# Kernel optimization log

Measured on AMD Instinct MI355X. Metric: run time of the kernel, lower is better.

The kernel has to match this reference:

```python
import jax, jax.numpy as jnp
import numpy as np

HEADS = 8


def setup_inputs() -> dict:
    key = jax.random.key(0)
    ks = jax.random.split(key, 6)
    dim = 256
    s = 0.02
    return {
        "x": jax.random.normal(ks[0], (8, dim, 32, 32), jnp.float32),
        "w_qkv": jax.random.normal(ks[1], (3 * dim, dim), jnp.float32) * s,
        "w_out": jax.random.normal(ks[2], (dim, dim), jnp.float32) * s,
        "b_out": jnp.zeros((dim,), jnp.float32),
        "w_g1": jax.random.normal(ks[3], (dim // 4, dim), jnp.float32) * s,
        "b_g1": jnp.zeros((dim // 4,), jnp.float32),
        "w_g2": jax.random.normal(ks[4], (1, dim // 4), jnp.float32) * s,
        "b_g2": jnp.zeros((1,), jnp.float32),
    }


def _conv1x1(t, w, bias=None):
    # 1x1 conv == channel matmul
    y = jnp.einsum('bchw,oc->bohw', t, w)
    if bias is not None:
        y = y + bias[None, :, None, None]
    return y


def _forward(x, w_qkv, w_out, b_out, w_g1, b_g1, w_g2, b_g2):
    b, c, h, w = x.shape
    heads = HEADS
    d = c // heads
    n = h * w
    m = min(h, w)
    scale = d ** (-0.5)

    qkv = _conv1x1(x, w_qkv)  # [b, 3c, h, w]

    def to_heads(t):  # 'b (h d) x y -> b h (x y) d'
        return t.reshape(b, heads, d, n).transpose(0, 1, 3, 2)

    q, k, v = (to_heads(t) for t in jnp.split(qkv, 3, axis=1))

    attn = jax.nn.softmax(jnp.einsum('bhid,bhjd->bhij', q, k) * scale, axis=-1)

    # diagonal branch (anti-diagonal scores are computed in the original but
    # never used in the output -> omitted as dead code)
    q2d = q.reshape(b, heads, h, w, d)
    k2d = k.reshape(b, heads, h, w, d)
    q_dm = jnp.diagonal(q2d, axis1=2, axis2=3)  # [b, heads, d, m]
    k_dm = jnp.diagonal(k2d, axis1=2, axis2=3)
    diag_main = jnp.einsum('bhnd,bhmd->bhnm', q_dm, k_dm) * scale  # [b, heads, d, d]
    diag_vec = jnp.diagonal(diag_main.mean(axis=1), axis1=-2, axis2=-1)  # [b, d]
    diag_vec = jnp.pad(diag_vec, ((0, 0), (0, n - m)))  # [b, n] (d == m)

    DIAG_WEIGHT = 0.3
    enhanced = attn + DIAG_WEIGHT * diag_vec[:, None, :, None]

    out = jnp.einsum('bhij,bhjd->bhid', enhanced, v)  # [b, heads, n, d]
    out = out.reshape(b, heads, h, w, d).transpose(0, 1, 4, 2, 3).reshape(b, c, h, w)

    # left/right asymmetry gate
    mid = w // 2
    left = x[:, :, :, :mid]
    right = x[:, :, :, mid:]
    asym = jnp.abs(left - right[:, :, :, ::-1])  # [b, c, h, w/2]
    # adaptive_avg_pool2d (h, w/2) -> (h, w) with even w == width repeat by 2
    pooled = jnp.repeat(asym, 2, axis=3)
    g = _conv1x1(pooled, w_g1, b_g1)
    g = jax.nn.gelu(g, approximate=False)
    g = jax.nn.sigmoid(_conv1x1(g, w_g2, b_g2))  # [b, 1, h, w]

    out = out * (1.0 + g)
    return _conv1x1(out, w_out, b_out)


def reference(x, w_qkv, w_out, b_out, w_g1, b_g1, w_g2, b_g2):
    return _forward(x, w_qkv, w_out, b_out, w_g1, b_g1, w_g2, b_g2)
```

## Files before the change

kernel.cpp:

```cpp
#include <hip/hip_runtime.h>
#include <hip/hip_bf16.h>
#include <math.h>

#define B 8
#define C 256
#define HEADS 8
#define D 32
#define NPIX 1024
#define OC 768
#define SCALE 0.17677669529663687f
#define LOG2E 1.4426950408889634f

typedef unsigned int uint;
typedef unsigned short u16;
typedef __attribute__((ext_vector_type(8))) short bf16x8;
typedef __attribute__((ext_vector_type(4))) short bf16x4;
typedef __attribute__((ext_vector_type(4))) float f32x4;

static __device__ inline u16 f2bf(float f) {
  uint u = __float_as_uint(f);
  return (u16)((u + 0x7fffu + ((u >> 16) & 1u)) >> 16);
}
static __device__ inline float bfval(u16 v) { return __uint_as_float((uint)v << 16); }
static __device__ inline float bf_lo(uint u) { return __uint_as_float(u << 16); }
static __device__ inline float bf_hi(uint u) { return __uint_as_float(u & 0xffff0000u); }

static __device__ inline uint pk2(float lo, float hi) {
  union { __hip_bfloat162 h; uint u; } cv;
  cv.h = __float22bfloat162_rn(float2{lo, hi});
  return cv.u;
}

__global__ __launch_bounds__(256) void k_prep(
    const float* __restrict__ x, const float* __restrict__ wqkv,
    const float* __restrict__ wout,
    u16* __restrict__ WQ, u16* __restrict__ WO, u16* __restrict__ XT) {
  const int bid = blockIdx.x, t = threadIdx.x;
  __shared__ u16 tile[64][65];
  if (bid < 256) {
    const float* src;
    u16* dst;
    int base;
    if (bid < 192) { src = wqkv; dst = WQ; base = bid * 1024; }
    else           { src = wout; dst = WO; base = (bid - 192) * 1024; }
    float4 v = *(const float4*)(src + base + t * 4);
    uint2 pk = make_uint2((uint)f2bf(v.x) | ((uint)f2bf(v.y) << 16),
                          (uint)f2bf(v.z) | ((uint)f2bf(v.w) << 16));
    *(uint2*)(dst + base + t * 4) = pk;
    return;
  }
  const int id = bid - 256;
  const int pt = id & 15, ct = (id >> 4) & 3, b = id >> 6;
  {
    const int px = t & 63, cq = t >> 6;
    const float* xb = x + ((size_t)(b * C + ct * 64)) * NPIX + pt * 64;
#pragma unroll
    for (int m = 0; m < 16; ++m) {
      const int c = cq * 16 + m;
      tile[c][px] = f2bf(xb[(size_t)c * NPIX + px]);
    }
  }
  __syncthreads();
  {
    const int cc = t & 63, pq = t >> 6;
    const int c = ct * 64 + cc;
    const int kc = c >> 5, quad = (c >> 3) & 3, mm = c & 7;
    u16* dst = XT + ((size_t)((b * 64 + pt * 4 + pq) * 8 + kc) * 512 +
                     quad * 128 + mm);
#pragma unroll
    for (int m = 0; m < 16; ++m)
      dst[m * 8] = tile[cc][pq * 16 + m];
  }
}

__global__ __launch_bounds__(256) void k_qkv_mfma(
    const u16* __restrict__ XTF, const u16* __restrict__ WQ,
    u16* __restrict__ Q, u16* __restrict__ Kk, u16* __restrict__ VT) {
  const int ob = blockIdx.x, pb = blockIdx.y, b = blockIdx.z;
  const int wv = threadIdx.x >> 6, lane = threadIdx.x & 63;
  const int quad = lane >> 4, l15 = lane & 15;
  const int part = ob >> 2;
  const int odl = (ob & 3) * 64 + wv * 16;
  const int hh = odl >> 5, d0 = odl & 31;
  const int bh = b * HEADS + hh;
  const int pix0 = pb * 128;

  const u16* arow = WQ + (size_t)(ob * 64 + wv * 16 + l15) * C;
  bf16x8 af[8];
#pragma unroll
  for (int kc = 0; kc < 8; ++kc)
    af[kc] = *(const bf16x8*)(arow + kc * 32 + quad * 8);

  const u16* xb = XTF + (size_t)(b * 64 + pb * 8) * 8 * 512 + lane * 8;
  f32x4 acc[8];
#pragma unroll
  for (int nt = 0; nt < 8; ++nt) acc[nt] = (f32x4){0.f, 0.f, 0.f, 0.f};

  for (int kc = 0; kc < 8; ++kc) {
#pragma unroll
    for (int nt = 0; nt < 8; ++nt) {
      bf16x8 bfr = *(const bf16x8*)(xb + (size_t)(nt * 8 + kc) * 512);
      acc[nt] = __builtin_amdgcn_mfma_f32_16x16x32_bf16(af[kc], bfr, acc[nt], 0, 0, 0);
    }
  }

  if (part == 0) {
    const float qs = SCALE * LOG2E;
    u16* dst = Q + (size_t)bh * NPIX * D;
#pragma unroll
    for (int nt = 0; nt < 8; ++nt) {
      const int pix = pix0 + nt * 16 + l15;
      uint2 pk = make_uint2(
          (uint)f2bf(acc[nt][0] * qs) | ((uint)f2bf(acc[nt][1] * qs) << 16),
          (uint)f2bf(acc[nt][2] * qs) | ((uint)f2bf(acc[nt][3] * qs) << 16));
      *(uint2*)(dst + (size_t)pix * D + d0 + 4 * quad) = pk;
    }
  } else if (part == 1) {
    u16* kfb = Kk + (size_t)bh * NPIX * D;
    const int lane_k8 = (((d0 >> 3) + (quad >> 1)) * 16 + l15) * 8 + (quad & 1) * 4;
#pragma unroll
    for (int nt = 0; nt < 8; ++nt) {
      uint2 pk = make_uint2(
          (uint)f2bf(acc[nt][0]) | ((uint)f2bf(acc[nt][1]) << 16),
          (uint)f2bf(acc[nt][2]) | ((uint)f2bf(acc[nt][3]) << 16));
      *(uint2*)(kfb + (size_t)(pb * 8 + nt) * 512 + lane_k8) = pk;
    }
  } else {
    u16* vb = VT + (size_t)bh * NPIX * D;
#pragma unroll
    for (int nt = 0; nt < 8; ++nt) {
      const int pix = pix0 + nt * 16 + l15;
      const int jb16 = pix >> 4, qa = (pix >> 2) & 3, m = pix & 3;
#pragma unroll
      for (int r = 0; r < 4; ++r) {
        const int d = d0 + 4 * quad + r;
        const int nta = d >> 4, l15a = d & 15;
        vb[((size_t)(jb16 * 2 + nta) * 64 + qa * 16 + l15a) * 4 + m] =
            f2bf(acc[nt][r]);
      }
    }
  }
}

__global__ __launch_bounds__(256) void k_red(
    const u16* __restrict__ Q, const u16* __restrict__ KF,
    const u16* __restrict__ VT, float* __restrict__ diagv,
    float* __restrict__ colsum) {
  const int bid = blockIdx.x, tid = threadIdx.x;
  __shared__ float red[256];
  if (bid < 8) {
    const int b = bid;
    const int hh = tid >> 5, dd = tid & 31;
    const u16* qb = Q + (size_t)(b * HEADS + hh) * NPIX * D;
    const u16* kb = KF + (size_t)(b * HEADS + hh) * NPIX * D;
    float s = 0.f;
#pragma unroll 4
    for (int t = 0; t < 32; ++t) {
      const int j = t * 33;
      float qv = bfval(qb[(size_t)j * D + dd]);
      float kv = bfval(kb[(size_t)(j >> 4) * 512 +
                          ((dd >> 3) * 16 + (j & 15)) * 8 + (dd & 7)]);
      s += qv * kv;
    }
    red[tid] = s;
    __syncthreads();
    if (tid < 32) {
      float v = 0.f;
#pragma unroll
      for (int h8 = 0; h8 < 8; ++h8) v += red[h8 * 32 + tid];
      diagv[b * 32 + tid] = v * (0.125f / LOG2E);
    }
  } else {
    const int bh = bid - 8;
    const int d = tid >> 3, sl = tid & 7;
    const int nta = d >> 4, l15a = d & 15;
    const u16* vb = VT + (size_t)bh * NPIX * D;
    float s = 0.f;
    for (int jb = 0; jb < 8; ++jb) {
      const int jb16 = sl * 8 + jb;
#pragma unroll
      for (int qa = 0; qa < 4; ++qa) {
        const uint2 u = *(const uint2*)(
            vb + ((size_t)(jb16 * 2 + nta) * 64 + qa * 16 + l15a) * 4);
        s += bf_lo(u.x) + bf_hi(u.x) + bf_lo(u.y) + bf_hi(u.y);
      }
    }
    red[tid] = s;
    __syncthreads();
    if (tid < 32) {
      float v = 0.f;
#pragma unroll
      for (int g = 0; g < 8; ++g) v += red[tid * 8 + g];
      colsum[bh * D + tid] = v;
    }
  }
}

__global__ __launch_bounds__(512, 4) void k_attn(
    const u16* __restrict__ Q, const u16* __restrict__ KF,
    const u16* __restrict__ VF, const float* __restrict__ diagv,
    const float* __restrict__ colsum, u16* __restrict__ AOT) {
  const int qc = blockIdx.x;
  const int bh = blockIdx.y;
  const int b = bh >> 3, hh = bh & 7;
  const int wv = threadIdx.x >> 6, lane = threadIdx.x & 63;
  const int quad = lane >> 4, l15 = lane & 15;
  const int i0 = qc * 128 + wv * 16;

  __shared__ u16 sbuf[2][4096];

  const u16* Qb  = Q  + (size_t)bh * NPIX * D;
  const u16* KFb = KF + (size_t)bh * NPIX * D;
  const u16* VFb = VF + (size_t)bh * NPIX * D;

  bf16x8 qfrag = *(const bf16x8*)(Qb + (size_t)(i0 + l15) * D + quad * 8);

  f32x4 oacc[2];
  oacc[0] = (f32x4){0.f, 0.f, 0.f, 0.f};
  oacc[1] = (f32x4){0.f, 0.f, 0.f, 0.f};
  float lacc[4] = {};

  const int soff = (wv >= 4 ? 2048 : 0) + (wv & 3) * 512 + lane * 8;
  const u16* gsrc = (wv < 4 ? KFb : VFb) + (wv & 3) * 512 + lane * 8;
  u16* ldst[2] = { &sbuf[0][soff], &sbuf[1][soff] };

  *(uint4*)(ldst[0]) = *(const uint4*)(gsrc);
  __syncthreads();

  int cur = 0;
  for (int it = 0; it < 16; ++it) {
    if (it < 15)
      *(uint4*)(ldst[cur ^ 1]) = *(const uint4*)(gsrc + (size_t)(it + 1) * 2048);
    const u16* sK = &sbuf[cur][0];
    const u16* sV = &sbuf[cur][2048];

    f32x4 st[4];
#pragma unroll
    for (int jt = 0; jt < 4; ++jt) {
      bf16x8 kfrag = *(const bf16x8*)(sK + jt * 512 + lane * 8);
      st[jt] = __builtin_amdgcn_mfma_f32_16x16x32_bf16(
          kfrag, qfrag, (f32x4){0.f, 0.f, 0.f, 0.f}, 0, 0, 0);
    }

#pragma unroll
    for (int jt = 0; jt < 4; ++jt)
#pragma unroll
      for (int r = 0; r < 4; ++r) {
        float pv = exp2f(fminf(st[jt][r], 80.f));
        lacc[r] += pv;
        st[jt][r] = pv;
      }

    __builtin_amdgcn_s_setprio(1);
#pragma unroll
    for (int jt = 0; jt < 4; ++jt) {
      union { uint u[2]; bf16x4 v; } pa;
      pa.u[0] = pk2(st[jt][0], st[jt][1]);
      pa.u[1] = pk2(st[jt][2], st[jt][3]);
#pragma unroll
      for (int nt = 0; nt < 2; ++nt) {
        bf16x4 vfr = *(const bf16x4*)(sV + (jt * 2 + nt) * 256 + lane * 4);
        oacc[nt] = __builtin_amdgcn_mfma_f32_16x16x16bf16_1k(
            pa.v, vfr, oacc[nt], 0, 0, 0);
      }
    }
    __builtin_amdgcn_s_setprio(0);

    __syncthreads();
    cur ^= 1;
  }

  float lt = (lacc[0] + lacc[1]) + (lacc[2] + lacc[3]);
  lt += __shfl_xor(lt, 16, 64);
  lt += __shfl_xor(lt, 32, 64);
  const float linv = 1.f / lt;
  float rinv[4];
#pragma unroll
  for (int r = 0; r < 4; ++r) rinv[r] = __shfl(linv, quad * 4 + r, 64);

  const bool do_diag = (i0 < 32);
#pragma unroll
  for (int nt = 0; nt < 2; ++nt) {
    const int dch = hh * 32 + nt * 16 + l15;
    float cs = do_diag ? colsum[bh * D + (nt * 16 + l15)] : 0.f;
#pragma unroll
    for (int r = 0; r < 4; ++r) {
      const int irow = i0 + quad * 4 + r;
      float o = oacc[nt][r] * rinv[r];
      if (do_diag) o += 0.3f * diagv[b * 32 + irow] * cs;
      AOT[((size_t)b * NPIX + irow) * C + dch] = f2bf(o);
    }
  }
}

__global__ __launch_bounds__(256) void k_gate(
    const float* __restrict__ x,
    const float* __restrict__ wg1, const float* __restrict__ bg1,
    const float* __restrict__ wg2, const float* __restrict__ bg2,
    float* __restrict__ gate) {
  const int h = blockIdx.x, b = blockIdx.y, tid = threadIdx.x;
  __shared__ float pl[16 * 257];
  __shared__ float gl[16 * 65];

  {
    const int c = tid;
    const float* row = x + ((size_t)(b * C + c) * NPIX + h * 32);
    float v[32];
#pragma unroll
    for (int m = 0; m < 32; ++m) v[m] = row[m];
#pragma unroll
    for (int k = 0; k < 16; ++k) pl[k * 257 + c] = fabsf(v[k] - v[31 - k]);
  }
  __syncthreads();

  const int o16 = tid >> 4, k = tid & 15;
#pragma unroll 1
  for (int p = 0; p < 4; ++p) {
    const int o = p * 16 + o16;
    const float* wr = wg1 + o * C;
    float a0 = 0.f, a1 = 0.f, a2 = 0.f, a3 = 0.f;
#pragma unroll 4
    for (int c = 0; c < C; c += 4) {
      a0 += wr[c]     * pl[k * 257 + c];
      a1 += wr[c + 1] * pl[k * 257 + c + 1];
      a2 += wr[c + 2] * pl[k * 257 + c + 2];
      a3 += wr[c + 3] * pl[k * 257 + c + 3];
    }
    float a = bg1[o] + ((a0 + a1) + (a2 + a3));
    gl[k * 65 + o] = 0.5f * a * (1.f + erff(a * 0.70710678118654752f));
  }
  __syncthreads();

  if (tid < 16) {
    float s = bg2[0];
    for (int o = 0; o < 64; ++o)
      s += wg2[o] * gl[tid * 65 + o];
    gate[(b * 32 + h) * 16 + tid] = 1.f / (1.f + expf(-s));
  }
}

__global__ __launch_bounds__(256) void k_out_mfma(
    const u16* __restrict__ AOT, const u16* __restrict__ WO,
    const float* __restrict__ bout, const float* __restrict__ gate,
    float* __restrict__ out) {
  const int ob = blockIdx.x, pb = blockIdx.y, b = blockIdx.z;
  const int wv = threadIdx.x >> 6, lane = threadIdx.x & 63;
  const int quad = lane >> 4, l15 = lane & 15;
  const int o0 = ob * 64 + wv * 16;
  const int pix0 = pb * 128;

  const u16* arow = WO + (size_t)(o0 + l15) * C;
  bf16x8 af[8];
#pragma unroll
  for (int kc = 0; kc < 8; ++kc)
    af[kc] = *(const bf16x8*)(arow + kc * 32 + quad * 8);

  const u16* ab = AOT + (size_t)(b * NPIX + pix0) * C;
  f32x4 acc[8];
#pragma unroll
  for (int nt = 0; nt < 8; ++nt) acc[nt] = (f32x4){0.f, 0.f, 0.f, 0.f};

  for (int kc = 0; kc < 8; ++kc) {
#pragma unroll
    for (int nt = 0; nt < 8; ++nt) {
      bf16x8 bfr = *(const bf16x8*)(ab + (size_t)(nt * 16 + l15) * C +
                                    kc * 32 + quad * 8);
      acc[nt] = __builtin_amdgcn_mfma_f32_16x16x32_bf16(af[kc], bfr, acc[nt], 0, 0, 0);
    }
  }

#pragma unroll
  for (int nt = 0; nt < 8; ++nt) {
    const int pix = pix0 + nt * 16 + l15;
    const float gf = 1.f + gate[(b * 32 + (pix >> 5)) * 16 + ((pix & 31) >> 1)];
#pragma unroll
    for (int r = 0; r < 4; ++r) {
      const int o = o0 + 4 * quad + r;
      out[((size_t)b * C + o) * NPIX + pix] = acc[nt][r] * gf + bout[o];
    }
  }
}

extern "C" void kernel_launch(void* const* d_in, const int* in_sizes, int n_in,
                              void* d_out, int out_size, void* d_ws, size_t ws_size,
                              hipStream_t stream) {
  const float* x    = (const float*)d_in[0];
  const float* wqkv = (const float*)d_in[1];
  const float* wout = (const float*)d_in[2];
  const float* bout = (const float*)d_in[3];
  const float* wg1  = (const float*)d_in[4];
  const float* bg1  = (const float*)d_in[5];
  const float* wg2  = (const float*)d_in[6];
  const float* bg2  = (const float*)d_in[7];
  float* out = (float*)d_out;

  const size_t SZ = (size_t)B * HEADS * NPIX * D;
  u16* XT = (u16*)d_ws;
  u16* WQ = XT + SZ;
  u16* WO = WQ + (size_t)OC * C;
  u16* Q  = WO + (size_t)C * C;
  u16* Kq = Q + SZ;
  u16* VT = Kq + SZ;
  float* DIAG = (float*)(VT + SZ);
  float* COL  = DIAG + 256;
  float* GATE = COL + 2048;
  u16* AOT = XT;

  hipLaunchKernelGGL(k_prep, dim3(768), dim3(256), 0, stream,
                     x, wqkv, wout, WQ, WO, XT);
  hipLaunchKernelGGL(k_qkv_mfma, dim3(12, 8, B), dim3(256), 0, stream,
                     XT, WQ, Q, Kq, VT);
  hipLaunchKernelGGL(k_red, dim3(72), dim3(256), 0, stream,
                     Q, Kq, VT, DIAG, COL);
  hipLaunchKernelGGL(k_attn, dim3(8, 64), dim3(512), 0, stream,
                     Q, Kq, VT, DIAG, COL, AOT);
  hipLaunchKernelGGL(k_gate, dim3(32, B), dim3(256), 0, stream,
                     x, wg1, bg1, wg2, bg2, GATE);
  hipLaunchKernelGGL(k_out_mfma, dim3(4, 8, B), dim3(256), 0, stream,
                     AOT, WO, bout, GATE, out);
}
```

Baseline: 156.4 us.

## Fuse gate computation into prep kernel and write attention output in MFMA fragment layout

The gate kernel is merged into the prep kernel as an extra 256 blocks, removing one launch and letting gate work overlap with the weight conversion and transpose. The attention kernel now stores its bf16 output directly in the MFMA-fragment-tiled layout, so the output projection loads each fragment as one contiguous 16-byte read per lane instead of strided row reads. The attention output stores become scattered 2-byte writes, and the prep kernel's shared-memory footprint grows to the gate's size.

Measured after the change: 147.8 us. 5.5% less time.

```diff
diff --git a/kernel.cpp b/kernel.cpp
--- a/kernel.cpp
+++ b/kernel.cpp
@@ -31,12 +31,15 @@
   return cv.u;
 }
 
-__global__ __launch_bounds__(256) void k_prep(
+__global__ __launch_bounds__(256) void k_prep_gate(
     const float* __restrict__ x, const float* __restrict__ wqkv,
     const float* __restrict__ wout,
-    u16* __restrict__ WQ, u16* __restrict__ WO, u16* __restrict__ XT) {
+    const float* __restrict__ wg1, const float* __restrict__ bg1,
+    const float* __restrict__ wg2, const float* __restrict__ bg2,
+    u16* __restrict__ WQ, u16* __restrict__ WO, u16* __restrict__ XT,
+    float* __restrict__ gate) {
   const int bid = blockIdx.x, t = threadIdx.x;
-  __shared__ u16 tile[64][65];
+  __shared__ float smem[16 * 257 + 16 * 65];
   if (bid < 256) {
     const float* src;
     u16* dst;
@@ -49,27 +52,70 @@
     *(uint2*)(dst + base + t * 4) = pk;
     return;
   }
-  const int id = bid - 256;
-  const int pt = id & 15, ct = (id >> 4) & 3, b = id >> 6;
+  if (bid < 768) {
+    u16 (*tile)[65] = (u16(*)[65])smem;
+    const int id = bid - 256;
+    const int pt = id & 15, ct = (id >> 4) & 3, b = id >> 6;
+    {
+      const int px = t & 63, cq = t >> 6;
+      const float* xb = x + ((size_t)(b * C + ct * 64)) * NPIX + pt * 64;
+#pragma unroll
+      for (int m = 0; m < 16; ++m) {
+        const int c = cq * 16 + m;
+        tile[c][px] = f2bf(xb[(size_t)c * NPIX + px]);
+      }
+    }
+    __syncthreads();
+    {
+      const int cc = t & 63, pq = t >> 6;
+      const int c = ct * 64 + cc;
+      const int kc = c >> 5, quad = (c >> 3) & 3, mm = c & 7;
+      u16* dst = XT + ((size_t)((b * 64 + pt * 4 + pq) * 8 + kc) * 512 +
+                       quad * 128 + mm);
+#pragma unroll
+      for (int m = 0; m < 16; ++m)
+        dst[m * 8] = tile[cc][pq * 16 + m];
+    }
+    return;
+  }
+  const int id = bid - 768;
+  const int h = id & 31, b = id >> 5;
+  float* pl = smem;
+  float* gl = smem + 16 * 257;
   {
-    const int px = t & 63, cq = t >> 6;
-    const float* xb = x + ((size_t)(b * C + ct * 64)) * NPIX + pt * 64;
-#pragma unroll
-    for (int m = 0; m < 16; ++m) {
-      const int c = cq * 16 + m;
-      tile[c][px] = f2bf(xb[(size_t)c * NPIX + px]);
-    }
+    const int c = t;
+    const float* row = x + ((size_t)(b * C + c) * NPIX + h * 32);
+    float v[32];
+#pragma unroll
+    for (int m = 0; m < 32; ++m) v[m] = row[m];
+#pragma unroll
+    for (int k = 0; k < 16; ++k) pl[k * 257 + c] = fabsf(v[k] - v[31 - k]);
   }
   __syncthreads();
-  {
-    const int cc = t & 63, pq = t >> 6;
-    const int c = ct * 64 + cc;
-    const int kc = c >> 5, quad = (c >> 3) & 3, mm = c & 7;
-    u16* dst = XT + ((size_t)((b * 64 + pt * 4 + pq) * 8 + kc) * 512 +
-                     quad * 128 + mm);
-#pragma unroll
-    for (int m = 0; m < 16; ++m)
-      dst[m * 8] = tile[cc][pq * 16 + m];
+
+  const int o16 = t >> 4, k = t & 15;
+#pragma unroll 1
+  for (int p = 0; p < 4; ++p) {
+    const int o = p * 16 + o16;
+    const float* wr = wg1 + o * C;
+    float a0 = 0.f, a1 = 0.f, a2 = 0.f, a3 = 0.f;
+#pragma unroll 4
+    for (int c = 0; c < C; c += 4) {
+      a0 += wr[c]     * pl[k * 257 + c];
+      a1 += wr[c + 1] * pl[k * 257 + c + 1];
+      a2 += wr[c + 2] * pl[k * 257 + c + 2];
+      a3 += wr[c + 3] * pl[k * 257 + c + 3];
+    }
+    float a = bg1[o] + ((a0 + a1) + (a2 + a3));
+    gl[k * 65 + o] = 0.5f * a * (1.f + erff(a * 0.70710678118654752f));
+  }
+  __syncthreads();
+
+  if (t < 16) {
+    float s = bg2[0];
+    for (int o = 0; o < 64; ++o)
+      s += wg2[o] * gl[t * 65 + o];
+    gate[(b * 32 + h) * 16 + t] = 1.f / (1.f + expf(-s));
   }
 }
 
@@ -279,68 +325,25 @@
   for (int r = 0; r < 4; ++r) rinv[r] = __shfl(linv, quad * 4 + r, 64);
 
   const bool do_diag = (i0 < 32);
+  const int p16 = i0 >> 4;
+  u16* aobase = AOT + ((size_t)(b * 64 + p16) * 8 + hh) * 512 + (l15 & 7);
+  const int hi8 = l15 >> 3;
 #pragma unroll
   for (int nt = 0; nt < 2; ++nt) {
-    const int dch = hh * 32 + nt * 16 + l15;
+    const int qa = nt * 2 + hi8;
     float cs = do_diag ? colsum[bh * D + (nt * 16 + l15)] : 0.f;
 #pragma unroll
     for (int r = 0; r < 4; ++r) {
       const int irow = i0 + quad * 4 + r;
       float o = oacc[nt][r] * rinv[r];
       if (do_diag) o += 0.3f * diagv[b * 32 + irow] * cs;
-      AOT[((size_t)b * NPIX + irow) * C + dch] = f2bf(o);
-    }
-  }
-}
-
-__global__ __launch_bounds__(256) void k_gate(
-    const float* __restrict__ x,
-    const float* __restrict__ wg1, const float* __restrict__ bg1,
-    const float* __restrict__ wg2, const float* __restrict__ bg2,
-    float* __restrict__ gate) {
-  const int h = blockIdx.x, b = blockIdx.y, tid = threadIdx.x;
-  __shared__ float pl[16 * 257];
-  __shared__ float gl[16 * 65];
-
-  {
-    const int c = tid;
-    const float* row = x + ((size_t)(b * C + c) * NPIX + h * 32);
-    float v[32];
-#pragma unroll
-    for (int m = 0; m < 32; ++m) v[m] = row[m];
-#pragma unroll
-    for (int k = 0; k < 16; ++k) pl[k * 257 + c] = fabsf(v[k] - v[31 - k]);
-  }
-  __syncthreads();
-
-  const int o16 = tid >> 4, k = tid & 15;
-#pragma unroll 1
-  for (int p = 0; p < 4; ++p) {
-    const int o = p * 16 + o16;
-    const float* wr = wg1 + o * C;
-    float a0 = 0.f, a1 = 0.f, a2 = 0.f, a3 = 0.f;
-#pragma unroll 4
-    for (int c = 0; c < C; c += 4) {
-      a0 += wr[c]     * pl[k * 257 + c];
-      a1 += wr[c + 1] * pl[k * 257 + c + 1];
-      a2 += wr[c + 2] * pl[k * 257 + c + 2];
-      a3 += wr[c + 3] * pl[k * 257 + c + 3];
-    }
-    float a = bg1[o] + ((a0 + a1) + (a2 + a3));
-    gl[k * 65 + o] = 0.5f * a * (1.f + erff(a * 0.70710678118654752f));
-  }
-  __syncthreads();
-
-  if (tid < 16) {
-    float s = bg2[0];
-    for (int o = 0; o < 64; ++o)
-      s += wg2[o] * gl[tid * 65 + o];
-    gate[(b * 32 + h) * 16 + tid] = 1.f / (1.f + expf(-s));
+      aobase[(qa * 16 + quad * 4 + r) * 8] = f2bf(o);
+    }
   }
 }
 
 __global__ __launch_bounds__(256) void k_out_mfma(
-    const u16* __restrict__ AOT, const u16* __restrict__ WO,
+    const u16* __restrict__ AOF, const u16* __restrict__ WO,
     const float* __restrict__ bout, const float* __restrict__ gate,
     float* __restrict__ out) {
   const int ob = blockIdx.x, pb = blockIdx.y, b = blockIdx.z;
@@ -355,7 +358,7 @@
   for (int kc = 0; kc < 8; ++kc)
     af[kc] = *(const bf16x8*)(arow + kc * 32 + quad * 8);
 
-  const u16* ab = AOT + (size_t)(b * NPIX + pix0) * C;
+  const u16* ab = AOF + (size_t)(b * 64 + pb * 8) * 8 * 512 + lane * 8;
   f32x4 acc[8];
 #pragma unroll
   for (int nt = 0; nt < 8; ++nt) acc[nt] = (f32x4){0.f, 0.f, 0.f, 0.f};
@@ -363,8 +366,7 @@
   for (int kc = 0; kc < 8; ++kc) {
 #pragma unroll
     for (int nt = 0; nt < 8; ++nt) {
-      bf16x8 bfr = *(const bf16x8*)(ab + (size_t)(nt * 16 + l15) * C +
-                                    kc * 32 + quad * 8);
+      bf16x8 bfr = *(const bf16x8*)(ab + (size_t)(nt * 8 + kc) * 512);
       acc[nt] = __builtin_amdgcn_mfma_f32_16x16x32_bf16(af[kc], bfr, acc[nt], 0, 0, 0);
     }
   }
@@ -406,16 +408,14 @@
   float* GATE = COL + 2048;
   u16* AOT = XT;
 
-  hipLaunchKernelGGL(k_prep, dim3(768), dim3(256), 0, stream,
-                     x, wqkv, wout, WQ, WO, XT);
+  hipLaunchKernelGGL(k_prep_gate, dim3(1024), dim3(256), 0, stream,
+                     x, wqkv, wout, wg1, bg1, wg2, bg2, WQ, WO, XT, GATE);
   hipLaunchKernelGGL(k_qkv_mfma, dim3(12, 8, B), dim3(256), 0, stream,
                      XT, WQ, Q, Kq, VT);
   hipLaunchKernelGGL(k_red, dim3(72), dim3(256), 0, stream,
                      Q, Kq, VT, DIAG, COL);
   hipLaunchKernelGGL(k_attn, dim3(8, 64), dim3(512), 0, stream,
                      Q, Kq, VT, DIAG, COL, AOT);
-  hipLaunchKernelGGL(k_gate, dim3(32, B), dim3(256), 0, stream,
-                     x, wg1, bg1, wg2, bg2, GATE);
   hipLaunchKernelGGL(k_out_mfma, dim3(4, 8, B), dim3(256), 0, stream,
                      AOT, WO, bout, GATE, out);
 }
```
